# Kernel tuning notes

Hardware: AMD Instinct MI355X
Metric: run time of the kernel (lower is better)

## Reference

```python
import jax, jax.numpy as jnp
import numpy as np

B, C_IN, N_NODES = 512, 128, 511  # padded node axis = N_NODES + 1 (index 0 is the zero vector)


def setup_inputs() -> dict:
    key = jax.random.key(0)
    ks = jax.random.split(key, 8)
    trees = jax.random.normal(ks[0], (B, C_IN, N_NODES + 1), dtype=jnp.float32)
    idxes = jax.random.randint(ks[1], (B, 3 * N_NODES, 1), 0, N_NODES + 1, dtype=jnp.int64)

    def init_conv(k, out_c, in_c):
        kw, kb = jax.random.split(k)
        s = 1.0 / np.sqrt(in_c * 3)
        W = jax.random.uniform(kw, (out_c, in_c, 3), minval=-s, maxval=s, dtype=jnp.float32)
        b = jax.random.uniform(kb, (out_c,), minval=-s, maxval=s, dtype=jnp.float32)
        return W, b

    def init_lin(k, out_c, in_c):
        kw, kb = jax.random.split(k)
        s = 1.0 / np.sqrt(in_c)
        W = jax.random.uniform(kw, (out_c, in_c), minval=-s, maxval=s, dtype=jnp.float32)
        b = jax.random.uniform(kb, (out_c,), minval=-s, maxval=s, dtype=jnp.float32)
        return W, b

    W1, b1 = init_conv(ks[2], 256, C_IN)
    W2, b2 = init_conv(ks[3], 128, 256)
    W3, b3 = init_conv(ks[4], 64, 128)
    Wf1, bf1 = init_lin(ks[5], 32, 64)
    Wf2, bf2 = init_lin(ks[6], 1, 32)
    return dict(trees=trees, idxes=idxes, W1=W1, b1=b1, W2=W2, b2=b2,
                W3=W3, b3=b3, Wf1=Wf1, bf1=bf1, Wf2=Wf2, bf2=bf2)


def _tree_conv(x, idx, W, b):
    # x: [B, C, N+1], idx: [B, 3N] -> gather (self,left,right) triples, conv1d k=3 s=3
    Bs, C, _ = x.shape
    g = jnp.take_along_axis(x, jnp.broadcast_to(idx[:, None, :], (Bs, C, idx.shape[1])), axis=2)
    g = g.reshape(Bs, C, -1, 3)  # [B, C, N, 3]
    out = jnp.einsum('bcnk,ock->bon', g, W) + b[None, :, None]  # [B, O, N]
    zero = jnp.zeros((Bs, out.shape[1], 1), out.dtype)
    return jnp.concatenate([zero, out], axis=2)  # re-add zero-padding node at idx 0


def _tree_norm(x):
    # torch.std is unbiased (ddof=1); normalize over (channel, node) dims per tree
    mean = jnp.mean(x, axis=(1, 2), keepdims=True)
    n = x.shape[1] * x.shape[2]
    var = jnp.sum((x - mean) ** 2, axis=(1, 2), keepdims=True) / (n - 1)
    return (x - mean) / (jnp.sqrt(var) + 1e-5)


def _leaky(x):
    return jnp.where(x >= 0, x, 0.01 * x)


def reference(trees, idxes, W1, b1, W2, b2, W3, b3, Wf1, bf1, Wf2, bf2):
    idx = idxes[..., 0]  # [B, 3N]
    x = _leaky(_tree_norm(_tree_conv(trees, idx, W1, b1)))
    x = _leaky(_tree_norm(_tree_conv(x, idx, W2, b2)))
    x = _tree_norm(_tree_conv(x, idx, W3, b3))
    pooled = jnp.max(x, axis=2)  # DynamicPooling -> [B, 64]
    h = _leaky(pooled @ Wf1.T + bf1)
    return h @ Wf2.T + bf2  # [B, 1]
```

## Files before the change

kernel.cpp:

```cpp
#include <hip/hip_runtime.h>

#define TRIP 1533

typedef __attribute__((ext_vector_type(8))) short bf16x8;
typedef __attribute__((ext_vector_type(4))) float f32x4;

__device__ __forceinline__ void split2(float a, float b, unsigned& h, unsigned& l) {
    unsigned ba = __float_as_uint(a), bb = __float_as_uint(b);
    unsigned ha = ba & 0xFFFF0000u, hb = bb & 0xFFFF0000u;
    float ra = a - __uint_as_float(ha);
    float rb = b - __uint_as_float(hb);
    h = (ba >> 16) | hb;
    l = (__float_as_uint(ra) >> 16) | (__float_as_uint(rb) & 0xFFFF0000u);
}

template<int CIN, int COUT>
__global__ void k_repackW(const float* __restrict__ W,
                          unsigned short* __restrict__ Hi, unsigned short* __restrict__ Lo) {
    int id = blockIdx.x * 256 + threadIdx.x;
    if (id >= 3 * CIN * COUT) return;
    int o = id / (3 * CIN), kk = id % (3 * CIN);
    int ks = kk / CIN, c = kk % CIN;
    float v = W[(o * CIN + c) * 3 + ks];
    unsigned b = __float_as_uint(v);
    unsigned h = b & 0xFFFF0000u;
    float r = v - __uint_as_float(h);
    Hi[id] = (unsigned short)(b >> 16);
    Lo[id] = (unsigned short)(__float_as_uint(r) >> 16);
}

__global__ void k_transpose(const float* __restrict__ in, float* __restrict__ out) {
    __shared__ float tl[64][129];
    int b = blockIdx.z, n0 = blockIdx.x * 64, t = threadIdx.x;
    int n = t & 63;
    for (int c = t >> 6; c < 128; c += 4)
        tl[n][c] = in[((size_t)b * 128 + c) * 512 + n0 + n];
    __syncthreads();
    int cq = t & 31;
    for (int nr = t >> 5; nr < 64; nr += 8) {
        float4 v = { tl[nr][cq*4+0], tl[nr][cq*4+1], tl[nr][cq*4+2], tl[nr][cq*4+3] };
        *(float4*)&out[((size_t)b * 512 + n0 + nr) * 128 + cq * 4] = v;
    }
}

__global__ void k_zero_row0(float* __restrict__ o1, float* __restrict__ o2, float* __restrict__ o3) {
    int b = blockIdx.x, t = threadIdx.x;
    if (t < 256) o1[(size_t)b * 512 * 256 + t] = 0.f;
    if (t < 128) o2[(size_t)b * 512 * 128 + t] = 0.f;
    if (t < 64)  o3[(size_t)b * 512 * 64  + t] = 0.f;
}

template<int CIN, int COUT, int OCH_T, bool NORM_IN>
__global__ __launch_bounds__(256) void k_convmfma(
    const float* __restrict__ xin, const int* __restrict__ idx,
    const unsigned short* __restrict__ WHi, const unsigned short* __restrict__ WLo,
    const float* __restrict__ bias, float* __restrict__ out,
    const float* __restrict__ sIn, float* __restrict__ sOut)
{
    constexpr int K  = 3 * CIN;
    constexpr int NK = K / 32;
    constexpr int N_ = OCH_T / 32;
    constexpr int OH = OCH_T / 2;

    __shared__ unsigned short Gh[128][40], Gl[128][40];
    __shared__ unsigned short Wh[OCH_T][40], Wl[OCH_T][40];
    __shared__ int   il[384];
    __shared__ float rs[4], rq[4];

    const int b    = blockIdx.z;
    const int och0 = blockIdx.y * OCH_T;
    const int n0   = 1 + blockIdx.x * 128;
    const int t    = threadIdx.x;
    const int lane = t & 63, wave = t >> 6;
    const int wm = wave >> 1, wn = wave & 1;
    const int l15 = lane & 15, l16 = lane >> 4;

    float mean = 0.f, inv = 1.f;
    if (NORM_IN) {
        float s = sIn[b * 2], ss = sIn[b * 2 + 1];
        const float nel = (float)(CIN * 512);
        float mu  = s / nel;
        float var = (ss - nel * mu * mu) / (nel - 1.f);
        mean = mu; inv = 1.f / (sqrtf(var) + 1e-5f);
    }

    for (int i = t; i < 384; i += 256) {
        int n = i / 3;
        il[i] = (n0 + n <= 511) ? idx[b * TRIP + 3 * (n0 - 1) + i] : 0;
    }

    f32x4 acc[4][N_] = {};

    const int nodeL = t >> 1;
    const int cb    = (t & 1) * 16;

    for (int ch = 0; ch < NK; ++ch) {
        const int kk0 = ch * 32;
        const int ks  = kk0 / CIN, c0 = kk0 % CIN;
        __syncthreads();

        {
            const float* src = &xin[((size_t)b * 512 + il[nodeL * 3 + ks]) * CIN + c0 + cb];
            #pragma unroll
            for (int i = 0; i < 4; ++i) {
                float4 v = *(const float4*)&src[i * 4];
                if (NORM_IN) {
                    v.x = (v.x - mean) * inv; v.x = v.x >= 0.f ? v.x : 0.01f * v.x;
                    v.y = (v.y - mean) * inv; v.y = v.y >= 0.f ? v.y : 0.01f * v.y;
                    v.z = (v.z - mean) * inv; v.z = v.z >= 0.f ? v.z : 0.01f * v.z;
                    v.w = (v.w - mean) * inv; v.w = v.w >= 0.f ? v.w : 0.01f * v.w;
                }
                unsigned h01, l01, h23, l23;
                split2(v.x, v.y, h01, l01);
                split2(v.z, v.w, h23, l23);
                *(uint2*)&Gh[nodeL][cb + i * 4] = make_uint2(h01, h23);
                *(uint2*)&Gl[nodeL][cb + i * 4] = make_uint2(l01, l23);
            }
        }
        for (int f = t; f < OCH_T * 4; f += 256) {
            int och = f >> 2, s = (f & 3) * 8;
            size_t g = (size_t)(och0 + och) * K + kk0 + s;
            *(uint4*)&Wh[och][s] = *(const uint4*)&WHi[g];
            *(uint4*)&Wl[och][s] = *(const uint4*)&WLo[g];
        }
        __syncthreads();

        bf16x8 Ah[4], Al[4], Bh[N_], Bl[N_];
        #pragma unroll
        for (int mi = 0; mi < 4; ++mi) {
            int nl = wm * 64 + mi * 16 + l15;
            Ah[mi] = *(const bf16x8*)&Gh[nl][l16 * 8];
            Al[mi] = *(const bf16x8*)&Gl[nl][l16 * 8];
        }
        #pragma unroll
        for (int ni = 0; ni < N_; ++ni) {
            int ol = wn * OH + ni * 16 + l15;
            Bh[ni] = *(const bf16x8*)&Wh[ol][l16 * 8];
            Bl[ni] = *(const bf16x8*)&Wl[ol][l16 * 8];
        }
        #pragma unroll
        for (int mi = 0; mi < 4; ++mi)
            #pragma unroll
            for (int ni = 0; ni < N_; ++ni) {
                acc[mi][ni] = __builtin_amdgcn_mfma_f32_16x16x32_bf16(Ah[mi], Bh[ni], acc[mi][ni], 0, 0, 0);
                acc[mi][ni] = __builtin_amdgcn_mfma_f32_16x16x32_bf16(Ah[mi], Bl[ni], acc[mi][ni], 0, 0, 0);
                acc[mi][ni] = __builtin_amdgcn_mfma_f32_16x16x32_bf16(Al[mi], Bh[ni], acc[mi][ni], 0, 0, 0);
            }
    }

    float lsum = 0.f, lss = 0.f;
    #pragma unroll
    for (int ni = 0; ni < N_; ++ni) {
        int ol = wn * OH + ni * 16 + l15;
        float bi = bias[och0 + ol];
        #pragma unroll
        for (int mi = 0; mi < 4; ++mi) {
            #pragma unroll
            for (int r = 0; r < 4; ++r) {
                int nl = wm * 64 + mi * 16 + l16 * 4 + r;
                int ng = n0 + nl;
                if (ng <= 511) {
                    float v = acc[mi][ni][r] + bi;
                    out[((size_t)b * 512 + ng) * COUT + och0 + ol] = v;
                    lsum += v; lss += v * v;
                }
            }
        }
    }

    #pragma unroll
    for (int off = 32; off > 0; off >>= 1) {
        lsum += __shfl_down(lsum, off);
        lss  += __shfl_down(lss, off);
    }
    if (lane == 0) { rs[wave] = lsum; rq[wave] = lss; }
    __syncthreads();
    if (t == 0) {
        atomicAdd(&sOut[b * 2],     rs[0] + rs[1] + rs[2] + rs[3]);
        atomicAdd(&sOut[b * 2 + 1], rq[0] + rq[1] + rq[2] + rq[3]);
    }
}

__global__ __launch_bounds__(256) void k_pool_fc(
    const float* __restrict__ x,
    const float* __restrict__ stats,
    const float* __restrict__ Wf1, const float* __restrict__ bf1,
    const float* __restrict__ Wf2, const float* __restrict__ bf2,
    float* __restrict__ outp)
{
    __shared__ float cm[4][64];
    __shared__ float pool[64];
    __shared__ float h[32];
    int b = blockIdx.x, t = threadIdx.x;
    int c = t & 63, g = t >> 6;
    float m = -1e30f;
    for (int n = 1 + g; n <= 511; n += 4)
        m = fmaxf(m, x[((size_t)b * 512 + n) * 64 + c]);
    cm[g][c] = m;
    __syncthreads();
    if (t < 64) {
        float mm = fmaxf(fmaxf(cm[0][t], cm[1][t]), fmaxf(cm[2][t], cm[3][t]));
        mm = fmaxf(mm, 0.f);
        float s = stats[b * 2], ss = stats[b * 2 + 1];
        const float nel = 64.f * 512.f;
        float mu  = s / nel;
        float var = (ss - nel * mu * mu) / (nel - 1.f);
        float inv = 1.f / (sqrtf(var) + 1e-5f);
        pool[t] = (mm - mu) * inv;
    }
    __syncthreads();
    if (t < 32) {
        float acc = bf1[t];
        for (int cc = 0; cc < 64; ++cc) acc += pool[cc] * Wf1[t * 64 + cc];
        h[t] = acc >= 0.f ? acc : 0.01f * acc;
    }
    __syncthreads();
    if (t == 0) {
        float acc = bf2[0];
        for (int j = 0; j < 32; ++j) acc += h[j] * Wf2[j];
        outp[b] = acc;
    }
}

extern "C" void kernel_launch(void* const* d_in, const int* in_sizes, int n_in,
                              void* d_out, int out_size, void* d_ws, size_t ws_size,
                              hipStream_t stream)
{
    const float* trees = (const float*)d_in[0];
    const int*   idx32 = (const int*)d_in[1];
    const float* W1  = (const float*)d_in[2];
    const float* b1  = (const float*)d_in[3];
    const float* W2  = (const float*)d_in[4];
    const float* b2  = (const float*)d_in[5];
    const float* W3  = (const float*)d_in[6];
    const float* b3  = (const float*)d_in[7];
    const float* Wf1 = (const float*)d_in[8];
    const float* bf1 = (const float*)d_in[9];
    const float* Wf2 = (const float*)d_in[10];
    const float* bf2 = (const float*)d_in[11];
    float* outp = (float*)d_out;
    char*  ws   = (char*)d_ws;

    float*          stats = (float*)ws;
    unsigned short* w1h = (unsigned short*)(ws + 12288);
    unsigned short* w1l = (unsigned short*)(ws + 208896);
    unsigned short* w2h = (unsigned short*)(ws + 405504);
    unsigned short* w2l = (unsigned short*)(ws + 602112);
    unsigned short* w3h = (unsigned short*)(ws + 798720);
    unsigned short* w3l = (unsigned short*)(ws + 847872);
    char* chunkBase = ws + 897024;
    float* s0 = stats, *s1 = stats + 1024, *s2 = stats + 2048;

    const size_t fixedB = 897024;
    int Bc = 512;
    while (Bc > 1 && fixedB + (size_t)Bc * 917504 > ws_size) Bc >>= 1;

    hipMemsetAsync(stats, 0, 12288, stream);
    k_repackW<128, 256><<<384, 256, 0, stream>>>(W1, w1h, w1l);
    k_repackW<256, 128><<<384, 256, 0, stream>>>(W2, w2h, w2l);
    k_repackW<128, 64><<<96, 256, 0, stream>>>(W3, w3h, w3l);

    float* t0   = (float*)chunkBase;
    float* out1 = (float*)(chunkBase + (size_t)Bc * 262144);
    float* out3 = (float*)(chunkBase + (size_t)Bc * 786432);

    for (int c0 = 0; c0 < 512; c0 += Bc) {
        const float* treesC = trees + (size_t)c0 * 128 * 512;
        const int*   idxC   = idx32 + (size_t)c0 * TRIP;

        k_transpose<<<dim3(8, 1, Bc), 256, 0, stream>>>(treesC, t0);
        k_convmfma<128, 256, 128, false><<<dim3(4, 2, Bc), 256, 0, stream>>>(
            t0, idxC, w1h, w1l, b1, out1, nullptr, s0 + c0 * 2);
        k_zero_row0<<<Bc, 256, 0, stream>>>(out1, t0, out3);
        k_convmfma<256, 128, 128, true><<<dim3(4, 1, Bc), 256, 0, stream>>>(
            out1, idxC, w2h, w2l, b2, t0, s0 + c0 * 2, s1 + c0 * 2);
        k_convmfma<128, 64, 64, true><<<dim3(4, 1, Bc), 256, 0, stream>>>(
            t0, idxC, w3h, w3l, b3, out3, s1 + c0 * 2, s2 + c0 * 2);
        k_pool_fc<<<Bc, 256, 0, stream>>>(out3, s2 + c0 * 2, Wf1, bf1, Wf2, bf2, outp + c0);
    }

    (void)in_sizes; (void)n_in; (void)out_size; (void)ws_size;
}
```

Baseline: 699.7 us.

## Fix conv output tile at 64 channels and register-prefetch next gather chunk

The tree-conv MFMA kernel now always computes 64 output channels per block, doubling the grid in the channel dimension for layers 1 and 2. It also sets launch bounds to 4 blocks per CU, keeps the three gather indices in registers instead of shared memory, and prefetches the next K-chunk's gathered activations and weights into registers while the current chunk is processed. The aim is to hide global gather latency and raise occupancy. In exchange, each input row is gathered and converted to split bf16 more times, since more blocks each redo the same gather, and register pressure goes up.

Measured after the change: 725.2 us. 1.04x slower.

```diff
diff --git a/kernel.cpp b/kernel.cpp
--- a/kernel.cpp
+++ b/kernel.cpp
@@ -50,8 +50,8 @@
     if (t < 64)  o3[(size_t)b * 512 * 64  + t] = 0.f;
 }
 
-template<int CIN, int COUT, int OCH_T, bool NORM_IN>
-__global__ __launch_bounds__(256) void k_convmfma(
+template<int CIN, int COUT, bool NORM_IN>
+__global__ __launch_bounds__(256, 4) void k_convmfma(
     const float* __restrict__ xin, const int* __restrict__ idx,
     const unsigned short* __restrict__ WHi, const unsigned short* __restrict__ WLo,
     const float* __restrict__ bias, float* __restrict__ out,
@@ -59,16 +59,13 @@
 {
     constexpr int K  = 3 * CIN;
     constexpr int NK = K / 32;
-    constexpr int N_ = OCH_T / 32;
-    constexpr int OH = OCH_T / 2;
 
     __shared__ unsigned short Gh[128][40], Gl[128][40];
-    __shared__ unsigned short Wh[OCH_T][40], Wl[OCH_T][40];
-    __shared__ int   il[384];
+    __shared__ unsigned short Wh[64][40],  Wl[64][40];
     __shared__ float rs[4], rq[4];
 
     const int b    = blockIdx.z;
-    const int och0 = blockIdx.y * OCH_T;
+    const int och0 = blockIdx.y * 64;
     const int n0   = 1 + blockIdx.x * 128;
     const int t    = threadIdx.x;
     const int lane = t & 63, wave = t >> 6;
@@ -84,48 +81,70 @@
         mean = mu; inv = 1.f / (sqrtf(var) + 1e-5f);
     }
 
-    for (int i = t; i < 384; i += 256) {
-        int n = i / 3;
-        il[i] = (n0 + n <= 511) ? idx[b * TRIP + 3 * (n0 - 1) + i] : 0;
-    }
-
-    f32x4 acc[4][N_] = {};
-
     const int nodeL = t >> 1;
     const int cb    = (t & 1) * 16;
+    int il0 = 0, il1 = 0, il2 = 0;
+    if (n0 + nodeL <= 511) {
+        const int* ip = &idx[b * TRIP + 3 * (n0 - 1 + nodeL)];
+        il0 = ip[0]; il1 = ip[1]; il2 = ip[2];
+    }
+    const float* rowBase = &xin[(size_t)b * 512 * CIN + cb];
+
+    const int wOch = t >> 2, wU = t & 3;
+    const unsigned short* wSrcH = &WHi[(size_t)(och0 + wOch) * K + wU * 8];
+    const unsigned short* wSrcL = &WLo[(size_t)(och0 + wOch) * K + wU * 8];
+
+    f32x4 acc[4][2] = {};
+
+    float4 g0, g1, g2, g3;
+    uint4  wrh, wrl;
+    {
+        const float* src = rowBase + (size_t)il0 * CIN;
+        g0 = *(const float4*)&src[0];  g1 = *(const float4*)&src[4];
+        g2 = *(const float4*)&src[8];  g3 = *(const float4*)&src[12];
+        wrh = *(const uint4*)&wSrcH[0];
+        wrl = *(const uint4*)&wSrcL[0];
+    }
 
     for (int ch = 0; ch < NK; ++ch) {
-        const int kk0 = ch * 32;
-        const int ks  = kk0 / CIN, c0 = kk0 % CIN;
         __syncthreads();
 
         {
-            const float* src = &xin[((size_t)b * 512 + il[nodeL * 3 + ks]) * CIN + c0 + cb];
-            #pragma unroll
-            for (int i = 0; i < 4; ++i) {
-                float4 v = *(const float4*)&src[i * 4];
-                if (NORM_IN) {
-                    v.x = (v.x - mean) * inv; v.x = v.x >= 0.f ? v.x : 0.01f * v.x;
-                    v.y = (v.y - mean) * inv; v.y = v.y >= 0.f ? v.y : 0.01f * v.y;
-                    v.z = (v.z - mean) * inv; v.z = v.z >= 0.f ? v.z : 0.01f * v.z;
-                    v.w = (v.w - mean) * inv; v.w = v.w >= 0.f ? v.w : 0.01f * v.w;
-                }
-                unsigned h01, l01, h23, l23;
-                split2(v.x, v.y, h01, l01);
-                split2(v.z, v.w, h23, l23);
-                *(uint2*)&Gh[nodeL][cb + i * 4] = make_uint2(h01, h23);
-                *(uint2*)&Gl[nodeL][cb + i * 4] = make_uint2(l01, l23);
+            float4 v0 = g0, v1 = g1, v2 = g2, v3 = g3;
+            if (NORM_IN) {
+                #define LKY(x) { x = (x - mean) * inv; x = x >= 0.f ? x : 0.01f * x; }
+                LKY(v0.x) LKY(v0.y) LKY(v0.z) LKY(v0.w)
+                LKY(v1.x) LKY(v1.y) LKY(v1.z) LKY(v1.w)
+                LKY(v2.x) LKY(v2.y) LKY(v2.z) LKY(v2.w)
+                LKY(v3.x) LKY(v3.y) LKY(v3.z) LKY(v3.w)
+                #undef LKY
             }
-        }
-        for (int f = t; f < OCH_T * 4; f += 256) {
-            int och = f >> 2, s = (f & 3) * 8;
-            size_t g = (size_t)(och0 + och) * K + kk0 + s;
-            *(uint4*)&Wh[och][s] = *(const uint4*)&WHi[g];
-            *(uint4*)&Wl[och][s] = *(const uint4*)&WLo[g];
+            uint4 H0, L0, H1, L1;
+            split2(v0.x, v0.y, H0.x, L0.x); split2(v0.z, v0.w, H0.y, L0.y);
+            split2(v1.x, v1.y, H0.z, L0.z); split2(v1.z, v1.w, H0.w, L0.w);
+            split2(v2.x, v2.y, H1.x, L1.x); split2(v2.z, v2.w, H1.y, L1.y);
+            split2(v3.x, v3.y, H1.z, L1.z); split2(v3.z, v3.w, H1.w, L1.w);
+            *(uint4*)&Gh[nodeL][cb]     = H0;
+            *(uint4*)&Gh[nodeL][cb + 8] = H1;
+            *(uint4*)&Gl[nodeL][cb]     = L0;
+            *(uint4*)&Gl[nodeL][cb + 8] = L1;
+            *(uint4*)&Wh[wOch][wU * 8]  = wrh;
+            *(uint4*)&Wl[wOch][wU * 8]  = wrl;
+        }
+
+        if (ch + 1 < NK) {
+            const int kk0n = (ch + 1) * 32;
+            const int ksn  = kk0n / CIN, c0n = kk0n % CIN;
+            const int node = ksn == 0 ? il0 : (ksn == 1 ? il1 : il2);
+            const float* src = rowBase + (size_t)node * CIN + c0n;
+            g0 = *(const float4*)&src[0];  g1 = *(const float4*)&src[4];
+            g2 = *(const float4*)&src[8];  g3 = *(const float4*)&src[12];
+            wrh = *(const uint4*)&wSrcH[kk0n];
+            wrl = *(const uint4*)&wSrcL[kk0n];
         }
         __syncthreads();
 
-        bf16x8 Ah[4], Al[4], Bh[N_], Bl[N_];
+        bf16x8 Ah[4], Al[4], Bh[2], Bl[2];
         #pragma unroll
         for (int mi = 0; mi < 4; ++mi) {
             int nl = wm * 64 + mi * 16 + l15;
@@ -133,15 +152,15 @@
             Al[mi] = *(const bf16x8*)&Gl[nl][l16 * 8];
         }
         #pragma unroll
-        for (int ni = 0; ni < N_; ++ni) {
-            int ol = wn * OH + ni * 16 + l15;
+        for (int ni = 0; ni < 2; ++ni) {
+            int ol = wn * 32 + ni * 16 + l15;
             Bh[ni] = *(const bf16x8*)&Wh[ol][l16 * 8];
             Bl[ni] = *(const bf16x8*)&Wl[ol][l16 * 8];
         }
         #pragma unroll
         for (int mi = 0; mi < 4; ++mi)
             #pragma unroll
-            for (int ni = 0; ni < N_; ++ni) {
+            for (int ni = 0; ni < 2; ++ni) {
                 acc[mi][ni] = __builtin_amdgcn_mfma_f32_16x16x32_bf16(Ah[mi], Bh[ni], acc[mi][ni], 0, 0, 0);
                 acc[mi][ni] = __builtin_amdgcn_mfma_f32_16x16x32_bf16(Ah[mi], Bl[ni], acc[mi][ni], 0, 0, 0);
                 acc[mi][ni] = __builtin_amdgcn_mfma_f32_16x16x32_bf16(Al[mi], Bh[ni], acc[mi][ni], 0, 0, 0);
@@ -150,8 +169,8 @@
 
     float lsum = 0.f, lss = 0.f;
     #pragma unroll
-    for (int ni = 0; ni < N_; ++ni) {
-        int ol = wn * OH + ni * 16 + l15;
+    for (int ni = 0; ni < 2; ++ni) {
+        int ol = wn * 32 + ni * 16 + l15;
         float bi = bias[och0 + ol];
         #pragma unroll
         for (int mi = 0; mi < 4; ++mi) {
@@ -269,12 +288,12 @@
         const int*   idxC   = idx32 + (size_t)c0 * TRIP;
 
         k_transpose<<<dim3(8, 1, Bc), 256, 0, stream>>>(treesC, t0);
-        k_convmfma<128, 256, 128, false><<<dim3(4, 2, Bc), 256, 0, stream>>>(
+        k_convmfma<128, 256, false><<<dim3(4, 4, Bc), 256, 0, stream>>>(
             t0, idxC, w1h, w1l, b1, out1, nullptr, s0 + c0 * 2);
         k_zero_row0<<<Bc, 256, 0, stream>>>(out1, t0, out3);
-        k_convmfma<256, 128, 128, true><<<dim3(4, 1, Bc), 256, 0, stream>>>(
+        k_convmfma<256, 128, true><<<dim3(4, 2, Bc), 256, 0, stream>>>(
             out1, idxC, w2h, w2l, b2, t0, s0 + c0 * 2, s1 + c0 * 2);
-        k_convmfma<128, 64, 64, true><<<dim3(4, 1, Bc), 256, 0, stream>>>(
+        k_convmfma<128, 64, true><<<dim3(4, 1, Bc), 256, 0, stream>>>(
             t0, idxC, w3h, w3l, b3, out3, s1 + c0 * 2, s2 + c0 * 2);
         k_pool_fc<<<Bc, 256, 0, stream>>>(out3, s2 + c0 * 2, Wf1, bf1, Wf2, bf2, outp + c0);
     }
```
